# Kernel optimization log

Measured on AMD Instinct MI355X. Metric: run time of the kernel, lower is better.

The kernel has to match this reference:

```python
import jax, jax.numpy as jnp
import numpy as np

N_NODES = 50000
NEG_SLOPE = 0.2


def setup_inputs() -> dict:
    key = jax.random.key(0)
    k1, k2, k3, k4 = jax.random.split(key, 4)
    N, E, F, H, C = 50000, 800000, 128, 4, 32
    x = jax.random.normal(k1, (N, F), dtype=jnp.float32)
    edge_index = jax.random.randint(k2, (2, E), 0, N, dtype=jnp.int32)
    weight = jax.random.normal(k3, (F, H * C), dtype=jnp.float32) * 0.1  # glorot-ish scale
    att = jax.random.normal(k4, (1, H, 2 * C), dtype=jnp.float32) * 0.1
    bias = jnp.zeros((C,), dtype=jnp.float32)
    return {"x": x, "edge_index": edge_index, "weight": weight, "att": att, "bias": bias}


def reference(x, edge_index, weight, att, bias):
    N = x.shape[0]
    H, C2 = att.shape[1], att.shape[2]
    C = C2 // 2
    # linear projection -> [N, H, C]
    xw = jnp.matmul(x, weight).reshape(N, H, C)
    row, col = edge_index[0], edge_index[1]
    # per-edge attention logits: gather both endpoints, concat along channel
    x_i = xw[row]                     # [E, H, C]
    x_j = xw[col]                     # [E, H, C]
    cat_x = jnp.concatenate([x_i, x_j], axis=-1)      # [E, H, 2C]
    alpha = jnp.sum(cat_x * att, axis=-1)             # [E, H]
    alpha = jnp.where(alpha >= 0, alpha, NEG_SLOPE * alpha)  # leaky_relu
    # segment softmax grouped by row (source index, as in the torch code)
    seg_max = jax.ops.segment_max(alpha, row, num_segments=N)
    seg_max = jnp.where(jnp.isfinite(seg_max), seg_max, 0.0)
    alpha = jnp.exp(alpha - seg_max[row])
    seg_sum = jax.ops.segment_sum(alpha, row, num_segments=N)
    alpha = alpha / (seg_sum[row] + 1e-16)            # [E, H]
    # PyG propagate: message = alpha * x_j where x_j = x[edge_index[0]],
    # aggregated (scatter-add) into target = edge_index[1]
    msg = alpha[..., None] * xw[row]                  # [E, H, C]
    out = jax.ops.segment_sum(msg, col, num_segments=N)  # [N, H, C]
    out = out.mean(axis=1) + bias                     # concat=False -> head mean, + bias
    return out
```

## Files before the change

kernel.cpp:

```cpp
#include <hip/hip_runtime.h>
#include <hip/hip_fp16.h>

#define FDIM 128
#define HEADS 4
#define CD 32
#define BM 64

typedef __attribute__((ext_vector_type(8))) short bfrag;
typedef __attribute__((ext_vector_type(4))) float ffrag;

static __device__ __forceinline__ unsigned short f2bf(float v) {
    unsigned u = __float_as_uint(v);
    u += 0x7FFF + ((u >> 16) & 1);
    return (unsigned short)(u >> 16);
}
static __device__ __forceinline__ float bf2f(unsigned short u) {
    return __uint_as_float(((unsigned)u) << 16);
}

__global__ __launch_bounds__(256) void k_wsplit(const float* __restrict__ w,
                                                unsigned short* __restrict__ wt_hi,
                                                unsigned short* __restrict__ wt_lo)
{
    int i = blockIdx.x * 256 + threadIdx.x;
    float v = w[i];
    unsigned short h = f2bf(v);
    float r = v - bf2f(h);
    int k = i >> 7, n = i & 127;
    wt_hi[n * FDIM + k] = h;
    wt_lo[n * FDIM + k] = f2bf(r);
}

__global__ __launch_bounds__(256) void k_gemm(const float* __restrict__ x,
                                              const unsigned short* __restrict__ wt_hi,
                                              const unsigned short* __restrict__ wt_lo,
                                              const float* __restrict__ att,
                                              unsigned short* __restrict__ xwh,
                                              float* __restrict__ a_src,
                                              float* __restrict__ a_dst,
                                              float4* __restrict__ zero_base,
                                              int nz4, int N)
{
    __shared__ float accs[BM * 132];
    __shared__ float attl[HEADS * 2 * CD];
    int t = threadIdx.x;
    int row0 = blockIdx.x * BM;
    for (int i = blockIdx.x * 256 + t; i < nz4; i += gridDim.x * 256)
        zero_base[i] = make_float4(0.f, 0.f, 0.f, 0.f);
    attl[t] = att[t];

    int l = t & 63, wv = t >> 6;
    int la = l & 15, lr = l >> 4;
    int arow = row0 + wv * 16 + la;
    bool aval = arow < N;
    const float* xbase = x + (size_t)arow * FDIM + lr * 8;

    ffrag acc[8] = {};
#pragma unroll
    for (int ks = 0; ks < 4; ks++) {
        float xv[8] = {0.f, 0.f, 0.f, 0.f, 0.f, 0.f, 0.f, 0.f};
        if (aval) {
            float4 f0 = *(const float4*)(xbase + ks * 32);
            float4 f1 = *(const float4*)(xbase + ks * 32 + 4);
            xv[0] = f0.x; xv[1] = f0.y; xv[2] = f0.z; xv[3] = f0.w;
            xv[4] = f1.x; xv[5] = f1.y; xv[6] = f1.z; xv[7] = f1.w;
        }
        bfrag ah, al;
#pragma unroll
        for (int j = 0; j < 8; j++) {
            unsigned short h = f2bf(xv[j]);
            ah[j] = (short)h;
            al[j] = (short)f2bf(xv[j] - bf2f(h));
        }
        int boff = ks * 32 + lr * 8;
#pragma unroll
        for (int ct = 0; ct < 8; ct++) {
            int o = (ct * 16 + la) * FDIM + boff;
            bfrag bh = *(const bfrag*)(wt_hi + o);
            bfrag bl = *(const bfrag*)(wt_lo + o);
            acc[ct] = __builtin_amdgcn_mfma_f32_16x16x32_bf16(ah, bh, acc[ct], 0, 0, 0);
            acc[ct] = __builtin_amdgcn_mfma_f32_16x16x32_bf16(ah, bl, acc[ct], 0, 0, 0);
            acc[ct] = __builtin_amdgcn_mfma_f32_16x16x32_bf16(al, bh, acc[ct], 0, 0, 0);
        }
    }

#pragma unroll
    for (int i = 0; i < 4; i++) {
        int r = row0 + wv * 16 + lr * 4 + i;
        if (r < N) {
            uint2 pa, pb;
            pa.x = (unsigned)f2bf(acc[0][i]) | ((unsigned)f2bf(acc[2][i]) << 16);
            pa.y = (unsigned)f2bf(acc[4][i]) | ((unsigned)f2bf(acc[6][i]) << 16);
            pb.x = (unsigned)f2bf(acc[1][i]) | ((unsigned)f2bf(acc[3][i]) << 16);
            pb.y = (unsigned)f2bf(acc[5][i]) | ((unsigned)f2bf(acc[7][i]) << 16);
            *(uint2*)&xwh[(size_t)r * FDIM + la * 4] = pa;
            *(uint2*)&xwh[(size_t)r * FDIM + 64 + la * 4] = pb;
        }
    }
#pragma unroll
    for (int ct = 0; ct < 8; ct++)
#pragma unroll
        for (int i = 0; i < 4; i++)
            accs[(wv * 16 + lr * 4 + i) * 132 + ct * 16 + la] = acc[ct][i];
    __syncthreads();
    int row = t >> 2, h = t & 3;
    const float* ap = &attl[h * 2 * CD];
    const float* xr = &accs[row * 132 + h * CD];
    float s = 0.f, d = 0.f;
#pragma unroll 8
    for (int c = 0; c < CD; c++) { float v = xr[c]; s += v * ap[c]; d += v * ap[CD + c]; }
    int n = row0 + row;
    if (n < N) { a_src[n * 4 + h] = s; a_dst[n * 4 + h] = d; }
}

__global__ __launch_bounds__(256) void k_esum(const int* __restrict__ ei, int E,
                                              const float* __restrict__ a_src,
                                              const float* __restrict__ a_dst,
                                              float* __restrict__ seg,
                                              __half* __restrict__ ealpha)
{
    int gid = blockIdx.x * 256 + threadIdx.x;
    if (gid >= E * HEADS) return;
    int e = gid >> 2, h = gid & 3;
    int r = ei[e], cl = ei[E + e];
    float a = a_src[r * 4 + h] + a_dst[cl * 4 + h];
    a = a >= 0.f ? a : 0.2f * a;
    float ex = __expf(a);
    ealpha[gid] = __float2half(ex);
    atomicAdd(&seg[r * 4 + h], ex);
}

__global__ __launch_bounds__(256) void k_scatter(const int* __restrict__ ei, int E,
                                                 const __half* __restrict__ ealpha,
                                                 const float* __restrict__ seg,
                                                 const unsigned short* __restrict__ xwh,
                                                 __half2* __restrict__ out_acc2)
{
    int t = threadIdx.x;
    int le = t >> 4, c2 = t & 15;
    int e = blockIdx.x * 16 + le;
    if (e >= E) return;
    int r = ei[e], cl = ei[E + e];
    int lane = t & 63;
    float av = 0.f;
    if (c2 < 4) av = 0.25f * __half2float(ealpha[e * 4 + c2]) / (seg[r * 4 + c2] + 1e-16f);
    uint4 q = ((const uint4*)(xwh + (size_t)r * FDIM))[c2];
    float a0 = __shfl(av, (lane & 48) + 0, 64);
    float a1 = __shfl(av, (lane & 48) + 1, 64);
    float a2 = __shfl(av, (lane & 48) + 2, 64);
    float a3 = __shfl(av, (lane & 48) + 3, 64);
    float v0 = a0 * bf2f((unsigned short)(q.x & 0xFFFF)) + a1 * bf2f((unsigned short)(q.x >> 16))
             + a2 * bf2f((unsigned short)(q.y & 0xFFFF)) + a3 * bf2f((unsigned short)(q.y >> 16));
    float v1 = a0 * bf2f((unsigned short)(q.z & 0xFFFF)) + a1 * bf2f((unsigned short)(q.z >> 16))
             + a2 * bf2f((unsigned short)(q.w & 0xFFFF)) + a3 * bf2f((unsigned short)(q.w >> 16));
    unsafeAtomicAdd(&out_acc2[(size_t)cl * 16 + c2], __floats2half2_rn(v0, v1));
}

__global__ void k_final(const __half2* __restrict__ out_acc2, const float4* __restrict__ bias,
                        float4* __restrict__ out, int N)
{
    int i = blockIdx.x * 256 + threadIdx.x;
    if (i >= N * 8) return;
    float4 b = bias[i & 7];
    float2 f0 = __half22float2(out_acc2[i * 2]);
    float2 f1 = __half22float2(out_acc2[i * 2 + 1]);
    out[i] = make_float4(f0.x + b.x, f0.y + b.y, f1.x + b.z, f1.y + b.w);
}

extern "C" void kernel_launch(void* const* d_in, const int* in_sizes, int n_in,
                              void* d_out, int out_size, void* d_ws, size_t ws_size,
                              hipStream_t stream)
{
    const float* x    = (const float*)d_in[0];
    const int*   ei   = (const int*)d_in[1];
    const float* w    = (const float*)d_in[2];
    const float* att  = (const float*)d_in[3];
    const float* bias = (const float*)d_in[4];
    float* out = (float*)d_out;
    int N = in_sizes[0] / FDIM;
    int E = in_sizes[1] / 2;

    unsigned short* xwh = (unsigned short*)d_ws;
    float* fws      = (float*)(xwh + (size_t)N * FDIM);
    float* a_src    = fws;
    float* a_dst    = a_src + (size_t)N * HEADS;
    float* seg      = a_dst + (size_t)N * HEADS;
    __half2* out_acc2 = (__half2*)(seg + (size_t)N * HEADS);
    __half* ealpha  = (__half*)(out_acc2 + (size_t)N * 16);
    unsigned short* wt_hi = (unsigned short*)(ealpha + (size_t)E * HEADS);
    unsigned short* wt_lo = wt_hi + FDIM * FDIM;

    int nz4 = N * 5;

    k_wsplit<<<(FDIM * FDIM) / 256, 256, 0, stream>>>(w, wt_hi, wt_lo);
    k_gemm<<<(N + BM - 1) / BM, 256, 0, stream>>>(x, wt_hi, wt_lo, att, xwh, a_src, a_dst,
                                                  (float4*)seg, nz4, N);
    k_esum<<<(E * HEADS + 255) / 256, 256, 0, stream>>>(ei, E, a_src, a_dst, seg, ealpha);
    k_scatter<<<(E + 15) / 16, 256, 0, stream>>>(ei, E, ealpha, seg, xwh, out_acc2);
    k_final<<<(N * 8 + 255) / 256, 256, 0, stream>>>(out_acc2, (const float4*)bias, (float4*)out, N);
}
```

Before: 210.0 us.

## Bucket edges by destination and aggregate in shared memory instead of global atomics

Adds a histogram and two-level scan that counting-sort the edges into 256 destination-node buckets. A new placement kernel computes the exp logits, adds them into the softmax denominators, and writes packed 16-byte records (src, dst, four half logits) into bucket order. The aggregate kernel then accumulates messages per bucket with fp32 shared-memory atomics, split four ways, and a final pass sums the four partials and adds the bias. This replaces the per-edge global half2 atomics, at the cost of extra launches, the record write and read, and a four-way partial-sum buffer.

```diff
diff --git a/kernel.cpp b/kernel.cpp
--- a/kernel.cpp
+++ b/kernel.cpp
@@ -5,6 +5,10 @@
 #define HEADS 4
 #define CD 32
 #define BM 64
+#define NBKT 256
+#define CHUNK 256
+#define SSUB 4
+#define MAXNL 200
 
 typedef __attribute__((ext_vector_type(8))) short bfrag;
 typedef __attribute__((ext_vector_type(4))) float ffrag;
@@ -29,6 +33,61 @@
     int k = i >> 7, n = i & 127;
     wt_hi[n * FDIM + k] = h;
     wt_lo[n * FDIM + k] = f2bf(r);
+}
+
+__global__ __launch_bounds__(256) void k_hist(const int* __restrict__ ei, int E, int N,
+                                              int* __restrict__ cnt)
+{
+    __shared__ int h[NBKT];
+    int t = threadIdx.x, chunk = blockIdx.x;
+    h[t] = 0;
+    __syncthreads();
+    int e = chunk * CHUNK + t;
+    if (e < E) atomicAdd(&h[(ei[E + e] * NBKT) / N], 1);
+    __syncthreads();
+    cnt[chunk * NBKT + t] = h[t];
+}
+
+__global__ __launch_bounds__(256) void k_scanA(const int* __restrict__ cnt,
+                                               int* __restrict__ boff,
+                                               int* __restrict__ btot, int nch)
+{
+    __shared__ int ws[4];
+    int t = threadIdx.x, lane = t & 63, w = t >> 6, b = blockIdx.x;
+    int carry = 0;
+    for (int c0 = 0; c0 < nch; c0 += 256) {
+        int idx = c0 + t;
+        int v = (idx < nch) ? cnt[idx * NBKT + b] : 0;
+        int x = v;
+#pragma unroll
+        for (int d = 1; d < 64; d <<= 1) { int y = __shfl_up(x, d, 64); if (lane >= d) x += y; }
+        if (lane == 63) ws[w] = x;
+        __syncthreads();
+        int woff = 0;
+        for (int i = 0; i < w; i++) woff += ws[i];
+        int tot = ws[0] + ws[1] + ws[2] + ws[3];
+        if (idx < nch) boff[b * nch + idx] = carry + woff + (x - v);
+        carry += tot;
+        __syncthreads();
+    }
+    if (t == 0) btot[b] = carry;
+}
+
+__global__ __launch_bounds__(256) void k_scanB(const int* __restrict__ btot,
+                                               int* __restrict__ bbase, int E)
+{
+    __shared__ int ws[4];
+    int t = threadIdx.x, lane = t & 63, w = t >> 6;
+    int v = btot[t];
+    int x = v;
+#pragma unroll
+    for (int d = 1; d < 64; d <<= 1) { int y = __shfl_up(x, d, 64); if (lane >= d) x += y; }
+    if (lane == 63) ws[w] = x;
+    __syncthreads();
+    int woff = 0;
+    for (int i = 0; i < w; i++) woff += ws[i];
+    bbase[t] = woff + (x - v);
+    if (t == 255) bbase[256] = E;
 }
 
 __global__ __launch_bounds__(256) void k_gemm(const float* __restrict__ x,
@@ -72,10 +131,10 @@
             ah[j] = (short)h;
             al[j] = (short)f2bf(xv[j] - bf2f(h));
         }
-        int boff = ks * 32 + lr * 8;
+        int boffk = ks * 32 + lr * 8;
 #pragma unroll
         for (int ct = 0; ct < 8; ct++) {
-            int o = (ct * 16 + la) * FDIM + boff;
+            int o = (ct * 16 + la) * FDIM + boffk;
             bfrag bh = *(const bfrag*)(wt_hi + o);
             bfrag bl = *(const bfrag*)(wt_lo + o);
             acc[ct] = __builtin_amdgcn_mfma_f32_16x16x32_bf16(ah, bh, acc[ct], 0, 0, 0);
@@ -113,58 +172,103 @@
     if (n < N) { a_src[n * 4 + h] = s; a_dst[n * 4 + h] = d; }
 }
 
-__global__ __launch_bounds__(256) void k_esum(const int* __restrict__ ei, int E,
-                                              const float* __restrict__ a_src,
-                                              const float* __restrict__ a_dst,
-                                              float* __restrict__ seg,
-                                              __half* __restrict__ ealpha)
-{
-    int gid = blockIdx.x * 256 + threadIdx.x;
-    if (gid >= E * HEADS) return;
-    int e = gid >> 2, h = gid & 3;
-    int r = ei[e], cl = ei[E + e];
-    float a = a_src[r * 4 + h] + a_dst[cl * 4 + h];
-    a = a >= 0.f ? a : 0.2f * a;
-    float ex = __expf(a);
-    ealpha[gid] = __float2half(ex);
-    atomicAdd(&seg[r * 4 + h], ex);
-}
-
-__global__ __launch_bounds__(256) void k_scatter(const int* __restrict__ ei, int E,
-                                                 const __half* __restrict__ ealpha,
-                                                 const float* __restrict__ seg,
-                                                 const unsigned short* __restrict__ xwh,
-                                                 __half2* __restrict__ out_acc2)
-{
+__global__ __launch_bounds__(256) void k_eplace(const int* __restrict__ ei, int E, int N,
+                                                const float* __restrict__ a_src,
+                                                const float* __restrict__ a_dst,
+                                                float* __restrict__ seg,
+                                                const int* __restrict__ boff,
+                                                const int* __restrict__ bbase,
+                                                unsigned* __restrict__ recs, int nch)
+{
+    __shared__ int sOff[NBKT];
+    __shared__ int lcnt[NBKT];
+    int t = threadIdx.x, chunk = blockIdx.x;
+    sOff[t] = bbase[t] + boff[t * nch + chunk];
+    lcnt[t] = 0;
+    __syncthreads();
+    int lane = t & 63, h = t & 3, gl = lane & ~3;
+#pragma unroll
+    for (int j = 0; j < CHUNK / 64; j++) {
+        int e = chunk * CHUNK + j * 64 + (t >> 2);
+        if (e < E) {
+            int r = ei[e], cl = ei[E + e];
+            float a = a_src[r * 4 + h] + a_dst[cl * 4 + h];
+            a = a >= 0.f ? a : 0.2f * a;
+            float ex = __expf(a);
+            atomicAdd(&seg[r * 4 + h], ex);
+            float e0 = __shfl(ex, gl + 0, 64);
+            float e1 = __shfl(ex, gl + 1, 64);
+            float e2 = __shfl(ex, gl + 2, 64);
+            float e3 = __shfl(ex, gl + 3, 64);
+            __half2 h01 = __floats2half2_rn(e0, e1);
+            __half2 h23 = __floats2half2_rn(e2, e3);
+            int pos = 0;
+            if (h == 0) {
+                int b2 = (cl * NBKT) / N;
+                pos = sOff[b2] + atomicAdd(&lcnt[b2], 1);
+            }
+            pos = __shfl(pos, gl, 64);
+            unsigned val = (h == 0) ? (unsigned)r
+                         : (h == 1) ? (unsigned)cl
+                         : (h == 2) ? *(unsigned*)&h01 : *(unsigned*)&h23;
+            recs[(size_t)pos * 4 + h] = val;
+        }
+    }
+}
+
+__global__ __launch_bounds__(256) void k_aggregate(const unsigned* __restrict__ recs,
+                                                   const int* __restrict__ bbase,
+                                                   const unsigned short* __restrict__ xwh,
+                                                   const float* __restrict__ seg,
+                                                   float* __restrict__ out_part, int N)
+{
+    __shared__ float lacc[MAXNL * 32];
     int t = threadIdx.x;
+    int b = blockIdx.x >> 2, s = blockIdx.x & 3;
+    int ln0 = (b * N + NBKT - 1) / NBKT;
+    int ln1 = ((b + 1) * N + NBKT - 1) / NBKT;
+    int NL = ln1 - ln0;
+    for (int i = t; i < NL * 32; i += 256) lacc[i] = 0.f;
+    __syncthreads();
+    int lo = bbase[b], hi = bbase[b + 1];
     int le = t >> 4, c2 = t & 15;
-    int e = blockIdx.x * 16 + le;
-    if (e >= E) return;
-    int r = ei[e], cl = ei[E + e];
-    int lane = t & 63;
-    float av = 0.f;
-    if (c2 < 4) av = 0.25f * __half2float(ealpha[e * 4 + c2]) / (seg[r * 4 + c2] + 1e-16f);
-    uint4 q = ((const uint4*)(xwh + (size_t)r * FDIM))[c2];
-    float a0 = __shfl(av, (lane & 48) + 0, 64);
-    float a1 = __shfl(av, (lane & 48) + 1, 64);
-    float a2 = __shfl(av, (lane & 48) + 2, 64);
-    float a3 = __shfl(av, (lane & 48) + 3, 64);
-    float v0 = a0 * bf2f((unsigned short)(q.x & 0xFFFF)) + a1 * bf2f((unsigned short)(q.x >> 16))
-             + a2 * bf2f((unsigned short)(q.y & 0xFFFF)) + a3 * bf2f((unsigned short)(q.y >> 16));
-    float v1 = a0 * bf2f((unsigned short)(q.z & 0xFFFF)) + a1 * bf2f((unsigned short)(q.z >> 16))
-             + a2 * bf2f((unsigned short)(q.w & 0xFFFF)) + a3 * bf2f((unsigned short)(q.w >> 16));
-    unsafeAtomicAdd(&out_acc2[(size_t)cl * 16 + c2], __floats2half2_rn(v0, v1));
-}
-
-__global__ void k_final(const __half2* __restrict__ out_acc2, const float4* __restrict__ bias,
+    for (int i = lo + s * 16 + le; i < hi; i += 64) {
+        uint4 rec = ((const uint4*)recs)[i];
+        int r = (int)rec.x, cl = (int)rec.y;
+        __half2 x01 = *(__half2*)&rec.z;
+        __half2 x23 = *(__half2*)&rec.w;
+        float4 sg = *(const float4*)&seg[r * 4];
+        float na0 = 0.25f * __low2float(x01) / (sg.x + 1e-16f);
+        float na1 = 0.25f * __high2float(x01) / (sg.y + 1e-16f);
+        float na2 = 0.25f * __low2float(x23) / (sg.z + 1e-16f);
+        float na3 = 0.25f * __high2float(x23) / (sg.w + 1e-16f);
+        uint4 q = ((const uint4*)(xwh + (size_t)r * FDIM))[c2];
+        float acc0 = na0 * bf2f((unsigned short)(q.x & 0xFFFF)) + na1 * bf2f((unsigned short)(q.x >> 16))
+                   + na2 * bf2f((unsigned short)(q.y & 0xFFFF)) + na3 * bf2f((unsigned short)(q.y >> 16));
+        float acc1 = na0 * bf2f((unsigned short)(q.z & 0xFFFF)) + na1 * bf2f((unsigned short)(q.z >> 16))
+                   + na2 * bf2f((unsigned short)(q.w & 0xFFFF)) + na3 * bf2f((unsigned short)(q.w >> 16));
+        int li = (cl - ln0) * 32 + c2 * 2;
+        atomicAdd(&lacc[li], acc0);
+        atomicAdd(&lacc[li + 1], acc1);
+    }
+    __syncthreads();
+    float* op = out_part + (size_t)s * N * 32 + (size_t)ln0 * 32;
+    for (int i = t; i < NL * 32; i += 256) op[i] = lacc[i];
+}
+
+__global__ void k_final(const float* __restrict__ out_part, const float4* __restrict__ bias,
                         float4* __restrict__ out, int N)
 {
     int i = blockIdx.x * 256 + threadIdx.x;
     if (i >= N * 8) return;
-    float4 b = bias[i & 7];
-    float2 f0 = __half22float2(out_acc2[i * 2]);
-    float2 f1 = __half22float2(out_acc2[i * 2 + 1]);
-    out[i] = make_float4(f0.x + b.x, f0.y + b.y, f1.x + b.z, f1.y + b.w);
+    size_t stride = (size_t)N * 8;
+    const float4* p = (const float4*)out_part;
+    float4 a = p[i], b1 = p[i + stride], c = p[i + 2 * stride], d = p[i + 3 * stride];
+    float4 bb = bias[i & 7];
+    out[i] = make_float4(a.x + b1.x + c.x + d.x + bb.x,
+                         a.y + b1.y + c.y + d.y + bb.y,
+                         a.z + b1.z + c.z + d.z + bb.z,
+                         a.w + b1.w + c.w + d.w + bb.w);
 }
 
 extern "C" void kernel_launch(void* const* d_in, const int* in_sizes, int n_in,
@@ -179,23 +283,31 @@
     float* out = (float*)d_out;
     int N = in_sizes[0] / FDIM;
     int E = in_sizes[1] / 2;
+    int nch = (E + CHUNK - 1) / CHUNK;
 
     unsigned short* xwh = (unsigned short*)d_ws;
-    float* fws      = (float*)(xwh + (size_t)N * FDIM);
-    float* a_src    = fws;
-    float* a_dst    = a_src + (size_t)N * HEADS;
-    float* seg      = a_dst + (size_t)N * HEADS;
-    __half2* out_acc2 = (__half2*)(seg + (size_t)N * HEADS);
-    __half* ealpha  = (__half*)(out_acc2 + (size_t)N * 16);
-    unsigned short* wt_hi = (unsigned short*)(ealpha + (size_t)E * HEADS);
+    uint4* recs  = (uint4*)(xwh + (size_t)N * FDIM);
+    float* seg   = (float*)(recs + (size_t)E);
+    unsigned short* wt_hi = (unsigned short*)(seg + (size_t)N * HEADS);
     unsigned short* wt_lo = wt_hi + FDIM * FDIM;
-
-    int nz4 = N * 5;
+    int* btot  = (int*)(wt_lo + FDIM * FDIM);
+    int* bbase = btot + NBKT;
+    int* cnt   = bbase + NBKT + 16;
+    int* boff  = cnt + (size_t)nch * NBKT;
+    float* a_src = (float*)(boff + (size_t)NBKT * nch);
+    float* a_dst = a_src + (size_t)N * HEADS;
+    float* out_part = (float*)cnt;
 
     k_wsplit<<<(FDIM * FDIM) / 256, 256, 0, stream>>>(w, wt_hi, wt_lo);
+    k_hist<<<nch, 256, 0, stream>>>(ei, E, N, cnt);
+    k_scanA<<<NBKT, 256, 0, stream>>>(cnt, boff, btot, nch);
+    k_scanB<<<1, 256, 0, stream>>>(btot, bbase, E);
     k_gemm<<<(N + BM - 1) / BM, 256, 0, stream>>>(x, wt_hi, wt_lo, att, xwh, a_src, a_dst,
-                                                  (float4*)seg, nz4, N);
-    k_esum<<<(E * HEADS + 255) / 256, 256, 0, stream>>>(ei, E, a_src, a_dst, seg, ealpha);
-    k_scatter<<<(E + 15) / 16, 256, 0, stream>>>(ei, E, ealpha, seg, xwh, out_acc2);
-    k_final<<<(N * 8 + 255) / 256, 256, 0, stream>>>(out_acc2, (const float4*)bias, (float4*)out, N);
-}
+                                                  (float4*)seg, N, N);
+    k_eplace<<<nch, 256, 0, stream>>>(ei, E, N, a_src, a_dst, seg, boff, bbase,
+                                      (unsigned*)recs, nch);
+    k_aggregate<<<NBKT * SSUB, 256, 0, stream>>>((const unsigned*)recs, bbase, xwh, seg,
+                                                 out_part, N);
+    k_final<<<(N * 8 + 255) / 256, 256, 0, stream>>>(out_part, (const float4*)bias,
+                                                     (float4*)out, N);
+}
```

After: 320.3 us. 52.6% more time.
